# Performance work log

Measured on AMD Instinct MI355X. Metric: run time of the kernel, lower is better.

Reference implementation:

```python
import jax, jax.numpy as jnp
import numpy as np

N = 8192
IN_F = 512
OUT_F = 128


def setup_inputs() -> dict:
    key = jax.random.key(0)
    k1, k2, k3, k4, k5, k6 = jax.random.split(key, 6)
    inp = jax.random.normal(k1, (N, IN_F), dtype=jnp.float32)
    adj = jax.random.randint(k2, (N, N), 0, 2).astype(jnp.float32)
    M = jax.random.uniform(k3, (N, N), dtype=jnp.float32)
    W = jax.random.normal(k4, (IN_F, OUT_F), dtype=jnp.float32) * (1.414 * np.sqrt(2.0 / (IN_F + OUT_F)))
    a_self = jax.random.normal(k5, (OUT_F, 1), dtype=jnp.float32) * (1.414 * np.sqrt(2.0 / (OUT_F + 1)))
    a_neighs = jax.random.normal(k6, (OUT_F, 1), dtype=jnp.float32) * (1.414 * np.sqrt(2.0 / (OUT_F + 1)))
    return {"input": inp, "adj": adj, "M": M, "W": W, "a_self": a_self, "a_neighs": a_neighs}


def reference(input, adj, M, W, a_self, a_neighs):
    h = input @ W                       # [N, OUT_F]
    attn_self = h @ a_self              # [N, 1]
    attn_neighs = h @ a_neighs          # [N, 1]
    e = attn_self + attn_neighs.T       # [N, N] broadcast add
    e = jax.nn.leaky_relu(e * M, negative_slope=0.2)
    e = jnp.where(adj > 0, e, jnp.float32(-9e15))
    attention = jax.nn.softmax(e, axis=1)
    h_prime = attention @ h             # [N, OUT_F]
    return jax.nn.elu(h_prime)          # concat=True
```

## Files before the change

kernel.cpp:

```cpp
#include <hip/hip_runtime.h>
#include <hip/hip_bf16.h>

typedef __attribute__((ext_vector_type(4))) float f32x4;
typedef __attribute__((ext_vector_type(8))) short s16x8;

constexpr int NN   = 8192;
constexpr int KIN  = 512;
constexpr int KOUT = 128;

constexpr int RBK  = 128;
constexpr int JC   = 4;
constexpr int JLEN = NN / JC;
constexpr int SGO  = 64;
constexpr int NS   = JLEN / SGO;
constexpr int SLABSZ = 16384;
constexpr int PBASE  = 32768;

__device__ __forceinline__ ushort f2bf(float x) {
    union { float f; unsigned u; } v; v.f = x;
    unsigned r = (v.u + 0x7fffu + ((v.u >> 16) & 1u)) >> 16;
    return (ushort)r;
}

__device__ __forceinline__ void gload_lds16(const void* g, void* l) {
    __builtin_amdgcn_global_load_lds((const __attribute__((address_space(1))) void*)g,
                                     (__attribute__((address_space(3))) void*)l, 16, 0, 0);
}

__global__ __launch_bounds__(256) void kA(const float* __restrict__ inp,
                                          const float* __restrict__ W,
                                          const float* __restrict__ a_s,
                                          const float* __restrict__ a_n,
                                          ushort* __restrict__ hT,
                                          float* __restrict__ s_out,
                                          float* __restrict__ t_out) {
    __shared__ float smem[16 * 512];
    const int t = threadIdx.x;
    const int rbase = blockIdx.x * 16;

#pragma unroll
    for (int it = 0; it < 8; ++it) {
        int idx = it * 256 + t;
        int r = idx >> 7;
        int c4 = (idx & 127) << 2;
        *(f32x4*)(&smem[r * 512 + c4]) =
            *(const f32x4*)(inp + (size_t)(rbase + r) * KIN + c4);
    }
    __syncthreads();

    const int c0 = (t & 31) * 4;
    const int rg = (t >> 5) * 2;
    float acc[2][4] = {};
#pragma unroll 4
    for (int k = 0; k < KIN; ++k) {
        f32x4 w4 = *(const f32x4*)(W + (size_t)k * KOUT + c0);
        float a0 = smem[(rg + 0) * 512 + k];
        float a1 = smem[(rg + 1) * 512 + k];
#pragma unroll
        for (int cc = 0; cc < 4; ++cc) {
            acc[0][cc] += a0 * w4[cc];
            acc[1][cc] += a1 * w4[cc];
        }
    }
    __syncthreads();

    float* h_lds = smem;
#pragma unroll
    for (int rr = 0; rr < 2; ++rr) {
        f32x4 v = {acc[rr][0], acc[rr][1], acc[rr][2], acc[rr][3]};
        *(f32x4*)(&h_lds[(rg + rr) * 128 + c0]) = v;
    }
    __syncthreads();

    {
        const int col = t >> 1;
        const int r0 = (t & 1) * 8;
        ushort tmp[8];
#pragma unroll
        for (int rr = 0; rr < 8; ++rr) tmp[rr] = f2bf(h_lds[(r0 + rr) * 128 + col]);
        *(f32x4*)(hT + (size_t)col * NN + rbase + r0) = *(f32x4*)&tmp[0];
    }

    {
        const int w = t >> 6, lane = t & 63;
        float as1 = a_s[lane], as2 = a_s[64 + lane];
        float an1 = a_n[lane], an2 = a_n[64 + lane];
#pragma unroll
        for (int rr = 0; rr < 4; ++rr) {
            int row = w * 4 + rr;
            float h1 = h_lds[row * 128 + lane];
            float h2 = h_lds[row * 128 + 64 + lane];
            float ps = h1 * as1 + h2 * as2;
            float pt = h1 * an1 + h2 * an2;
#pragma unroll
            for (int off = 32; off; off >>= 1) {
                ps += __shfl_xor(ps, off);
                pt += __shfl_xor(pt, off);
            }
            if (lane == 0) {
                s_out[rbase + row] = ps;
                t_out[rbase + row] = pt;
            }
        }
    }
}

__global__ __launch_bounds__(512, 1) void kH(const float* __restrict__ Mmat,
                                             const float* __restrict__ adjm,
                                             const ushort* __restrict__ hT,
                                             const float* __restrict__ s_in,
                                             const float* __restrict__ t_in,
                                             float* __restrict__ o_part,
                                             float* __restrict__ l_part) {
    __shared__ __align__(16) char LDS[49152];

    const int tid = threadIdx.x;
    const int w = tid >> 6;
    const int l = tid & 63;
    const int lrow = l & 15;
    const int kgrp = l >> 4;
    const int rb = blockIdx.x >> 2;
    const int jc = blockIdx.x & 3;
    const int j0 = jc * JLEN;
    const int row0 = rb * RBK;
    const int PH = (int)((blockIdx.x * 5u) & (unsigned)(NS - 1));
    const int POFF = PBASE + w * 2048;

    float sreg[4];
#pragma unroll
    for (int q = 0; q < 4; ++q) sreg[q] = s_in[row0 + w * 16 + q * 4 + (l >> 4)];
    float lsum4[4] = {0.f, 0.f, 0.f, 0.f};

    const float* Mq = Mmat + (size_t)(row0 + w * 16 + (l >> 4)) * NN + j0 + (l & 15) * 4;
    const float* Aq = adjm + (size_t)(row0 + w * 16 + (l >> 4)) * NN + j0 + (l & 15) * 4;
    const float* tq = t_in + j0 + (l & 15) * 4;

    const ushort* hq[2];
#pragma unroll
    for (int q2 = 0; q2 < 2; ++q2) {
        int r = w * 16 + q2 * 8 + (l >> 3);
        int sc = ((l & 7) ^ (r & 7)) * 8;
        hq[q2] = hT + (size_t)r * NN + j0 + sc;
    }

    f32x4 acc[8];
#pragma unroll
    for (int ct = 0; ct < 8; ++ct) acc[ct] = (f32x4){0.f, 0.f, 0.f, 0.f};

    f32x4 Mr[4], Ar[4], tr;

#define DMA_HT(P, SL)                                                            \
    _Pragma("unroll") for (int q2 = 0; q2 < 2; ++q2)                             \
        gload_lds16(hq[q2] + (size_t)(P) * SGO,                                  \
                    LDS + (SL) * SLABSZ + (w * 16 + q2 * 8) * 128);

#define LDG(P)                                                                   \
    _Pragma("unroll") for (int q = 0; q < 4; ++q) {                              \
        Mr[q] = *(const f32x4*)(Mq + (size_t)q * 4 * NN + (size_t)(P) * SGO);    \
        Ar[q] = *(const f32x4*)(Aq + (size_t)q * 4 * NN + (size_t)(P) * SGO);    \
    }                                                                            \
    tr = *(const f32x4*)(tq + (size_t)(P) * SGO);

#define EXPW_RELOAD(PN)                                                          \
    {                                                                            \
        _Pragma("unroll") for (int q = 0; q < 4; ++q) {                          \
            const int r = q * 4 + (l >> 4);                                      \
            float pv[4];                                                         \
            _Pragma("unroll") for (int e = 0; e < 4; ++e) {                      \
                float x = (sreg[q] + tr[e]) * Mr[q][e];                          \
                x = fmaxf(x, 0.2f * x);                                          \
                float p = __expf(x) * Ar[q][e];          \
                lsum4[q] += p;                                                   \
                pv[e] = p;                                                       \
            }                                                                    \
            uint2 u;                                                             \
            u.x = (unsigned)f2bf(pv[0]) | ((unsigned)f2bf(pv[1]) << 16);         \
            u.y = (unsigned)f2bf(pv[2]) | ((unsigned)f2bf(pv[3]) << 16);         \
            *(uint2*)(LDS + POFF + r * 128 + (((l & 15) * 8) ^ ((r & 7) << 4))) = u; \
            Mr[q] = *(const f32x4*)(Mq + (size_t)q * 4 * NN + (size_t)(PN) * SGO);   \
            Ar[q] = *(const f32x4*)(Aq + (size_t)q * 4 * NN + (size_t)(PN) * SGO);   \
        }                                                                        \
        tr = *(const f32x4*)(tq + (size_t)(PN) * SGO);                           \
    }

#define KSTEP(K, SL)                                                             \
    {                                                                            \
        s16x8 af = *(const s16x8*)(LDS + POFF + lrow * 128 +                     \
                                   ((((K) * 4 + kgrp) * 16) ^ ((lrow & 7) << 4))); \
        _Pragma("unroll") for (int ct = 0; ct < 8; ++ct) {                       \
            const int brow = ct * 16 + lrow;                                     \
            s16x8 bf = *(const s16x8*)(LDS + (SL) * SLABSZ + brow * 128 +        \
                                       ((((K) * 4 + kgrp) * 16) ^ ((lrow & 7) << 4))); \
            acc[ct] = __builtin_amdgcn_mfma_f32_16x16x32_bf16(af, bf, acc[ct], 0, 0, 0); \
        }                                                                        \
    }

    DMA_HT(PH, 0)
    LDG(PH)

#pragma unroll 1
    for (int s = 0; s < NS; ++s) {
        const int sl = s & 1;
        const int pn = (s + 1 + PH) & (NS - 1);
        asm volatile("s_waitcnt vmcnt(0)" ::: "memory");
        __builtin_amdgcn_s_barrier();
        asm volatile("" ::: "memory");
        DMA_HT(pn, sl ^ 1)
        EXPW_RELOAD(pn)
        KSTEP(0, sl)
        KSTEP(1, sl)
    }
#undef DMA_HT
#undef LDG
#undef EXPW_RELOAD
#undef KSTEP

#pragma unroll
    for (int q = 0; q < 4; ++q) {
        float v = lsum4[q];
#pragma unroll
        for (int off = 1; off < 16; off <<= 1) v += __shfl_xor(v, off);
        if ((l & 15) == 0)
            l_part[(size_t)jc * NN + row0 + w * 16 + q * 4 + (l >> 4)] = v;
    }

    float* op = o_part + (size_t)jc * NN * KOUT;
#pragma unroll
    for (int ct = 0; ct < 8; ++ct) {
#pragma unroll
        for (int r = 0; r < 4; ++r) {
            int gi = row0 + w * 16 + kgrp * 4 + r;
            int col = ct * 16 + lrow;
            op[(size_t)gi * KOUT + col] = acc[ct][r];
        }
    }
}

__global__ __launch_bounds__(256) void kC(const float* __restrict__ o_part,
                                          const float* __restrict__ l_part,
                                          float* __restrict__ out) {
    const int idx = blockIdx.x * 256 + threadIdx.x;
    const int i = idx >> 7;
    float osum = 0.f, lsum = 0.f;
#pragma unroll
    for (int p = 0; p < JC; ++p) {
        osum += o_part[(size_t)p * NN * KOUT + idx];
        lsum += l_part[(size_t)p * NN + i];
    }
    float v = osum / lsum;
    out[idx] = v > 0.f ? v : (__expf(v) - 1.f);
}

extern "C" void kernel_launch(void* const* d_in, const int* in_sizes, int n_in,
                              void* d_out, int out_size, void* d_ws, size_t ws_size,
                              hipStream_t stream) {
    const float* inp = (const float*)d_in[0];
    const float* adj = (const float*)d_in[1];
    const float* Mm  = (const float*)d_in[2];
    const float* W   = (const float*)d_in[3];
    const float* a_s = (const float*)d_in[4];
    const float* a_n = (const float*)d_in[5];
    float* out = (float*)d_out;

    char* ws = (char*)d_ws;
    ushort* hT    = (ushort*)(ws + 0);
    float*  s_buf = (float*)(ws + 2097152);
    float*  t_buf = (float*)(ws + 2129920);
    float*  l_prt = (float*)(ws + 2162688);
    float*  o_prt = (float*)(ws + 4194304);

    hipLaunchKernelGGL(kA, dim3(512), dim3(256), 0, stream, inp, W, a_s, a_n, hT, s_buf, t_buf);
    hipLaunchKernelGGL(kH, dim3(64 * JC), dim3(512), 0, stream, Mm, adj, hT, s_buf, t_buf, o_prt, l_prt);
    hipLaunchKernelGGL(kC, dim3(4096), dim3(256), 0, stream, o_prt, l_prt, out);
}
```

Baseline: 206.2 us.

## Deepen attention kernel pipeline to four register and LDS stages

Replaces the two-slab double-buffered loop with a four-stage software pipeline. M/adj/t register loads are issued three steps ahead and the hT DMA into LDS two steps ahead, with a partial vmcnt wait instead of vmcnt(0). LDS grows to 80 KB to hold four hT slabs, and the register footprint rises from one set of prefetch buffers to four. The goal is to hide HBM latency on the bandwidth-bound M/adj stream, at the cost of higher register pressure and spill risk.

Result: faster. 180.6 us (-12.4%).

```diff
diff --git a/kernel.cpp b/kernel.cpp
--- a/kernel.cpp
+++ b/kernel.cpp
@@ -14,7 +14,7 @@
 constexpr int SGO  = 64;
 constexpr int NS   = JLEN / SGO;
 constexpr int SLABSZ = 16384;
-constexpr int PBASE  = 32768;
+constexpr int PBASE  = 65536;
 
 __device__ __forceinline__ ushort f2bf(float x) {
     union { float f; unsigned u; } v; v.f = x;
@@ -105,14 +105,14 @@
     }
 }
 
-__global__ __launch_bounds__(512, 1) void kH(const float* __restrict__ Mmat,
+__global__ __launch_bounds__(512, 2) void kI(const float* __restrict__ Mmat,
                                              const float* __restrict__ adjm,
                                              const ushort* __restrict__ hT,
                                              const float* __restrict__ s_in,
                                              const float* __restrict__ t_in,
                                              float* __restrict__ o_part,
                                              float* __restrict__ l_part) {
-    __shared__ __align__(16) char LDS[49152];
+    __shared__ __align__(16) char LDS[81920];
 
     const int tid = threadIdx.x;
     const int w = tid >> 6;
@@ -126,6 +126,8 @@
     const int PH = (int)((blockIdx.x * 5u) & (unsigned)(NS - 1));
     const int POFF = PBASE + w * 2048;
 
+#define PCOL(S) ((((S) < NS ? (S) : NS - 1) + PH) & (NS - 1))
+
     float sreg[4];
 #pragma unroll
     for (int q = 0; q < 4; ++q) sreg[q] = s_in[row0 + w * 16 + q * 4 + (l >> 4)];
@@ -147,29 +149,34 @@
 #pragma unroll
     for (int ct = 0; ct < 8; ++ct) acc[ct] = (f32x4){0.f, 0.f, 0.f, 0.f};
 
-    f32x4 Mr[4], Ar[4], tr;
+    f32x4 Mr0[4], Ar0[4], tr0;
+    f32x4 Mr1[4], Ar1[4], tr1;
+    f32x4 Mr2[4], Ar2[4], tr2;
+    f32x4 Mr3[4], Ar3[4], tr3;
 
 #define DMA_HT(P, SL)                                                            \
     _Pragma("unroll") for (int q2 = 0; q2 < 2; ++q2)                             \
         gload_lds16(hq[q2] + (size_t)(P) * SGO,                                  \
                     LDS + (SL) * SLABSZ + (w * 16 + q2 * 8) * 128);
 
-#define LDG(P)                                                                   \
-    _Pragma("unroll") for (int q = 0; q < 4; ++q) {                              \
-        Mr[q] = *(const f32x4*)(Mq + (size_t)q * 4 * NN + (size_t)(P) * SGO);    \
-        Ar[q] = *(const f32x4*)(Aq + (size_t)q * 4 * NN + (size_t)(P) * SGO);    \
-    }                                                                            \
-    tr = *(const f32x4*)(tq + (size_t)(P) * SGO);
-
-#define EXPW_RELOAD(PN)                                                          \
+#define LDG(SL, P)                                                               \
+    {                                                                            \
+        _Pragma("unroll") for (int q = 0; q < 4; ++q) {                          \
+            Mr##SL[q] = *(const f32x4*)(Mq + (size_t)q * 4 * NN + (size_t)(P) * SGO); \
+            Ar##SL[q] = *(const f32x4*)(Aq + (size_t)q * 4 * NN + (size_t)(P) * SGO); \
+        }                                                                        \
+        tr##SL = *(const f32x4*)(tq + (size_t)(P) * SGO);                        \
+    }
+
+#define EXPW(SL)                                                                 \
     {                                                                            \
         _Pragma("unroll") for (int q = 0; q < 4; ++q) {                          \
             const int r = q * 4 + (l >> 4);                                      \
             float pv[4];                                                         \
             _Pragma("unroll") for (int e = 0; e < 4; ++e) {                      \
-                float x = (sreg[q] + tr[e]) * Mr[q][e];                          \
+                float x = (sreg[q] + tr##SL[e]) * Mr##SL[q][e];                  \
                 x = fmaxf(x, 0.2f * x);                                          \
-                float p = __expf(x) * Ar[q][e];          \
+                float p = __expf(x) * Ar##SL[q][e];      \
                 lsum4[q] += p;                                                   \
                 pv[e] = p;                                                       \
             }                                                                    \
@@ -177,10 +184,7 @@
             u.x = (unsigned)f2bf(pv[0]) | ((unsigned)f2bf(pv[1]) << 16);         \
             u.y = (unsigned)f2bf(pv[2]) | ((unsigned)f2bf(pv[3]) << 16);         \
             *(uint2*)(LDS + POFF + r * 128 + (((l & 15) * 8) ^ ((r & 7) << 4))) = u; \
-            Mr[q] = *(const f32x4*)(Mq + (size_t)q * 4 * NN + (size_t)(PN) * SGO);   \
-            Ar[q] = *(const f32x4*)(Aq + (size_t)q * 4 * NN + (size_t)(PN) * SGO);   \
         }                                                                        \
-        tr = *(const f32x4*)(tq + (size_t)(PN) * SGO);                           \
     }
 
 #define KSTEP(K, SL)                                                             \
@@ -195,25 +199,39 @@
         }                                                                        \
     }
 
-    DMA_HT(PH, 0)
-    LDG(PH)
+#define STAGE(C, D2, L3)                                                         \
+    {                                                                            \
+        const int s_ = s0 + (C);                                                 \
+        asm volatile("s_waitcnt vmcnt(20)" ::: "memory");                        \
+        __builtin_amdgcn_s_barrier();                                            \
+        asm volatile("" ::: "memory");                                           \
+        DMA_HT(PCOL(s_ + 2), D2)                                                 \
+        LDG(L3, PCOL(s_ + 3))                                                    \
+        EXPW(C)                                                                  \
+        KSTEP(0, C)                                                              \
+        KSTEP(1, C)                                                              \
+    }
+
+    LDG(0, PCOL(0))
+    DMA_HT(PCOL(0), 0)
+    LDG(1, PCOL(1))
+    DMA_HT(PCOL(1), 1)
+    LDG(2, PCOL(2))
 
 #pragma unroll 1
-    for (int s = 0; s < NS; ++s) {
-        const int sl = s & 1;
-        const int pn = (s + 1 + PH) & (NS - 1);
-        asm volatile("s_waitcnt vmcnt(0)" ::: "memory");
-        __builtin_amdgcn_s_barrier();
-        asm volatile("" ::: "memory");
-        DMA_HT(pn, sl ^ 1)
-        EXPW_RELOAD(pn)
-        KSTEP(0, sl)
-        KSTEP(1, sl)
-    }
+    for (int it = 0; it < NS / 4; ++it) {
+        const int s0 = it * 4;
+        STAGE(0, 2, 3)
+        STAGE(1, 3, 0)
+        STAGE(2, 0, 1)
+        STAGE(3, 1, 2)
+    }
+#undef STAGE
+#undef KSTEP
+#undef EXPW
+#undef LDG
 #undef DMA_HT
-#undef LDG
-#undef EXPW_RELOAD
-#undef KSTEP
+#undef PCOL
 
 #pragma unroll
     for (int q = 0; q < 4; ++q) {
@@ -270,6 +288,6 @@
     float*  o_prt = (float*)(ws + 4194304);
 
     hipLaunchKernelGGL(kA, dim3(512), dim3(256), 0, stream, inp, W, a_s, a_n, hT, s_buf, t_buf);
-    hipLaunchKernelGGL(kH, dim3(64 * JC), dim3(512), 0, stream, Mm, adj, hT, s_buf, t_buf, o_prt, l_prt);
+    hipLaunchKernelGGL(kI, dim3(64 * JC), dim3(512), 0, stream, Mm, adj, hT, s_buf, t_buf, o_prt, l_prt);
     hipLaunchKernelGGL(kC, dim3(4096), dim3(256), 0, stream, o_prt, l_prt, out);
 }
```
